# Performance work log

Hardware: AMD Instinct MI355X
Metric: run time of the kernel (lower is better)

## Reference

```python
import jax, jax.numpy as jnp
import numpy as np

NUMERICAL_STABILIZER = 1e-3  # Performer relu_kernel_transformation stabilizer


def _relu_kernel(x):
    # Performer ReLU kernel feature map (no random projection): relu(x) + eps.
    return jax.nn.relu(x) + NUMERICAL_STABILIZER


def setup_inputs() -> dict:
    key = jax.random.key(0)
    kq, kk, kv = jax.random.split(key, 3)
    B, L, D = 8, 32768, 64
    return {
        "queries": jax.random.normal(kq, (B, L, D), dtype=jnp.float32),
        "keys": jax.random.normal(kk, (B, L, D), dtype=jnp.float32),
        "values": jax.random.normal(kv, (B, L, D), dtype=jnp.float32),
        "top_k": 64,
    }


def reference(queries, keys, values, top_k):
    # Kernel feature maps (head dim of 1 in the original is a no-op squeeze).
    q_prime = _relu_kernel(queries)  # [B, L, D]
    k_prime = _relu_kernel(keys)     # [B, L, D]
    # ones[1,L] @ q_prime  ==  column sum over L  -> [B, D]
    reduced_q = jnp.sum(q_prime, axis=1)
    # scores[b, l] = reduced_q[b] . k_prime[b, l]   (attention column sums)
    scores = jnp.einsum("bd,bld->bl", reduced_q, k_prime)  # [B, L]
    # Cutoff = (top_k+1)-th largest score, matching sorted_idxs[:, top_k].
    cutoff = jax.lax.top_k(scores, top_k + 1)[0][:, top_k]  # [B]
    cond = scores > cutoff[:, None]                          # [B, L]
    return jnp.where(cond[:, :, None], values, jnp.zeros_like(values))
```

## Files before the change

kernel.cpp:

```cpp
#include <hip/hip_runtime.h>

#define BB 8
#define LL 32768
#define DD 64

typedef float f4 __attribute__((ext_vector_type(4)));
typedef unsigned long long u64x2 __attribute__((ext_vector_type(2)));


#define OUT_F4 (BB * LL * DD / 4)
#define CHUNKS_Q 64
#define ROWS_Q (LL / CHUNKS_Q)

__global__ __launch_bounds__(256) void k_reduce_q(const float* __restrict__ q,
                                                  double* __restrict__ part,
                                                  float* __restrict__ out) {
    {
        f4 z = (f4)(0.0f);
        f4* oz = (f4*)out + (size_t)blockIdx.x * 4096 + threadIdx.x;
#pragma unroll
        for (int i = 0; i < 16; ++i) oz[i * 256] = z;
    }

    int b     = blockIdx.x >> 6;
    int chunk = blockIdx.x & (CHUNKS_Q - 1);
    int quad  = threadIdx.x & 15;
    int rowg  = threadIdx.x >> 4;

    const f4* qb = (const f4*)(q + (size_t)b * LL * DD);
    const f4* base = qb + (size_t)(chunk * ROWS_Q + rowg) * 16 + quad;

    double a0 = 0.0, a1 = 0.0, a2 = 0.0, a3 = 0.0;
    f4 vb[8];
#pragma unroll
    for (int batch = 0; batch < 4; ++batch) {
#pragma unroll
        for (int j = 0; j < 8; ++j)
            vb[j] = base[(size_t)(batch * 8 + j) * 256];
#pragma unroll
        for (int j = 0; j < 8; ++j) {
            a0 += (double)fmaxf(vb[j].x, 0.0f) + 1e-3;
            a1 += (double)fmaxf(vb[j].y, 0.0f) + 1e-3;
            a2 += (double)fmaxf(vb[j].z, 0.0f) + 1e-3;
            a3 += (double)fmaxf(vb[j].w, 0.0f) + 1e-3;
        }
    }

    __shared__ double lds[16][16][5];
    lds[rowg][quad][0] = a0; lds[rowg][quad][1] = a1;
    lds[rowg][quad][2] = a2; lds[rowg][quad][3] = a3;
    __syncthreads();
    for (int s = 8; s > 0; s >>= 1) {
        if (rowg < s) {
            lds[rowg][quad][0] += lds[rowg + s][quad][0];
            lds[rowg][quad][1] += lds[rowg + s][quad][1];
            lds[rowg][quad][2] += lds[rowg + s][quad][2];
            lds[rowg][quad][3] += lds[rowg + s][quad][3];
        }
        __syncthreads();
    }
    if (rowg == 0) {
        double* pp = part + ((size_t)b * CHUNKS_Q + chunk) * DD;
        pp[quad * 4 + 0] = lds[0][quad][0];
        pp[quad * 4 + 1] = lds[0][quad][1];
        pp[quad * 4 + 2] = lds[0][quad][2];
        pp[quad * 4 + 3] = lds[0][quad][3];
    }
}

__global__ __launch_bounds__(256) void k_scores(const float* __restrict__ k,
                                                const double* __restrict__ part,
                                                double* __restrict__ scores,
                                                float* __restrict__ out) {
    __shared__ double s_part[4][DD];
    __shared__ double s_rq[DD];

    {
        f4 z = (f4)(0.0f);
        f4* oz = (f4*)out + (size_t)(OUT_F4 / 2)
               + (size_t)blockIdx.x * 2048 + threadIdx.x;
#pragma unroll
        for (int i = 0; i < 8; ++i) oz[i * 256] = z;
    }

    const int RPB = 256;
    int b     = blockIdx.x >> 7;
    int chunk = blockIdx.x & 127;

    {
        int d = threadIdx.x & 63;
        int g = threadIdx.x >> 6;
        const double* pp = part + (size_t)b * CHUNKS_Q * DD;
        double acc = 0.0;
#pragma unroll
        for (int j = 0; j < 16; ++j)
            acc += pp[(size_t)(g * 16 + j) * DD + d];
        s_part[g][d] = acc;
    }
    __syncthreads();
    if (threadIdx.x < DD) {
        int d = threadIdx.x;
        s_rq[d] = (s_part[0][d] + s_part[1][d]) + (s_part[2][d] + s_part[3][d]);
    }
    __syncthreads();

    int sub   = threadIdx.x & 15;
    int rowIn = threadIdx.x >> 4;

    double r0 = s_rq[sub * 4 + 0];
    double r1 = s_rq[sub * 4 + 1];
    double r2 = s_rq[sub * 4 + 2];
    double r3 = s_rq[sub * 4 + 3];

    const f4* kb = (const f4*)(k + (size_t)b * LL * DD);
    int l0 = chunk * RPB;
    const f4* base = kb + (size_t)(l0 + rowIn) * 16 + sub;

    f4 vb[8];
    double sv[8];
#pragma unroll
    for (int batch = 0; batch < 2; ++batch) {
#pragma unroll
        for (int i = 0; i < 8; ++i)
            vb[i] = base[(size_t)(batch * 8 + i) * 256];
#pragma unroll
        for (int i = 0; i < 8; ++i) {
            sv[i] = r0 * ((double)fmaxf(vb[i].x, 0.0f) + 1e-3)
                  + r1 * ((double)fmaxf(vb[i].y, 0.0f) + 1e-3)
                  + r2 * ((double)fmaxf(vb[i].z, 0.0f) + 1e-3)
                  + r3 * ((double)fmaxf(vb[i].w, 0.0f) + 1e-3);
        }
#pragma unroll
        for (int i = 0; i < 8; ++i) {
            double s = sv[i];
            s += __shfl_xor(s, 1, 16);
            s += __shfl_xor(s, 2, 16);
            s += __shfl_xor(s, 4, 16);
            s += __shfl_xor(s, 8, 16);
            if (sub == 0)
                scores[(size_t)b * LL + l0 + rowIn + 16 * (batch * 8 + i)] = s;
        }
    }
}

#define NCOPY 16
#define HSTRIDE 257
#define MAXSEL 96
__global__ __launch_bounds__(1024) void k_select_gather(const double* __restrict__ scores,
                                                        const int* __restrict__ topk_p,
                                                        const float* __restrict__ v,
                                                        float* __restrict__ out) {
    const int T = 1024;
    int b   = blockIdx.x;
    int tid = threadIdx.x;

    const u64x2* sb2 = (const u64x2*)(scores + (size_t)b * LL);

    unsigned long long myAnd = ~0ULL, myOr = 0ULL;
#pragma unroll
    for (int batch = 0; batch < 2; ++batch) {
        u64x2 p[8];
#pragma unroll
        for (int j = 0; j < 8; ++j) p[j] = sb2[tid + (batch * 8 + j) * T];
#pragma unroll
        for (int j = 0; j < 8; ++j) { myAnd &= p[j].x & p[j].y; myOr |= p[j].x | p[j].y; }
    }
    __shared__ unsigned long long sAnd[16], sOr[16];
#pragma unroll
    for (int off = 32; off >= 1; off >>= 1) {
        myAnd &= __shfl_down(myAnd, off);
        myOr  |= __shfl_down(myOr, off);
    }
    int wave = tid >> 6;
    if ((tid & 63) == 0) { sAnd[wave] = myAnd; sOr[wave] = myOr; }
    __syncthreads();
    __shared__ unsigned long long bAnd, bOr;
    __shared__ unsigned long long sh_prefix;
    __shared__ int sh_r, sh_digit, sh_newr, sh_cnt, sh_done, sh_ov, sh_cache_ok;
    __shared__ unsigned int hist[NCOPY * HSTRIDE];
    __shared__ unsigned int sWaveTot[4];
    if (tid == 0) {
        unsigned long long a = ~0ULL, o = 0ULL;
#pragma unroll
        for (int w = 0; w < 16; ++w) { a &= sAnd[w]; o |= sOr[w]; }
        bAnd = a; bOr = o;
        sh_prefix = 0ULL; sh_r = topk_p[0]; sh_done = 0; sh_cache_ok = 0;
    }
    __syncthreads();

    int copy = tid & (NCOPY - 1);
    unsigned long long m0 = 0, m1 = 0;
    int mcnt = 0;

    for (int shift = 56; shift >= 0; shift -= 8) {
        if (sh_done) break;

        unsigned int dA = (unsigned int)(bAnd >> shift) & 255u;
        unsigned int dO = (unsigned int)(bOr  >> shift) & 255u;
        if (dA == dO) {
            if (tid == 0) sh_prefix |= ((unsigned long long)dA << shift);
            __syncthreads();
            continue;
        }

        for (int i = tid; i < NCOPY * HSTRIDE; i += T) hist[i] = 0;
        if (tid == 0) sh_ov = 0;
        __syncthreads();

        int r = sh_r;
        unsigned long long prefix = sh_prefix;
        unsigned long long hm = (shift == 56) ? 0ULL : (~0ULL << (shift + 8));
        int usec = sh_cache_ok;

        if (usec) {
            if (mcnt >= 1) atomicAdd(&hist[copy * HSTRIDE + ((unsigned)(m0 >> shift) & 255u)], 1u);
            if (mcnt >= 2) atomicAdd(&hist[copy * HSTRIDE + ((unsigned)(m1 >> shift) & 255u)], 1u);
        } else {
            mcnt = 0;
#pragma unroll
            for (int batch = 0; batch < 2; ++batch) {
                u64x2 p[8];
#pragma unroll
                for (int j = 0; j < 8; ++j) p[j] = sb2[tid + (batch * 8 + j) * T];
#pragma unroll
                for (int j = 0; j < 8; ++j) {
                    unsigned long long ka = p[j].x, kb2 = p[j].y;
                    if ((ka & hm) == prefix) {
                        atomicAdd(&hist[copy * HSTRIDE + ((unsigned)(ka >> shift) & 255u)], 1u);
                        if (mcnt == 0) m0 = ka; else if (mcnt == 1) m1 = ka;
                        ++mcnt;
                    }
                    if ((kb2 & hm) == prefix) {
                        atomicAdd(&hist[copy * HSTRIDE + ((unsigned)(kb2 >> shift) & 255u)], 1u);
                        if (mcnt == 0) m0 = kb2; else if (mcnt == 1) m1 = kb2;
                        ++mcnt;
                    }
                }
            }
            if (mcnt > 2) sh_ov = 1;
        }
        __syncthreads();

        unsigned int suf = 0, sufn = 0;
        if (tid < 256) {
            unsigned int vtot = 0;
#pragma unroll
            for (int c = 0; c < NCOPY; ++c) vtot += hist[c * HSTRIDE + tid];
            unsigned int vv = vtot;
            int lane = tid & 63;
#pragma unroll
            for (int off = 1; off < 64; off <<= 1) {
                unsigned int t = __shfl_down(vv, off);
                if (lane + off < 64) vv += t;
            }
            if (lane == 0) sWaveTot[tid >> 6] = vv;
            suf = vv;
        }
        __syncthreads();
        if (tid < 256) {
            int lane = tid & 63, w = tid >> 6;
            unsigned int add = 0;
#pragma unroll
            for (int ww = 0; ww < 4; ++ww)
                if (ww > w) add += sWaveTot[ww];
            unsigned int nsuf = __shfl_down(suf, 1);
            suf += add;
            sufn = ((lane == 63) ? 0u : nsuf) + add;
            if (suf > (unsigned int)r && sufn <= (unsigned int)r) {
                sh_digit = tid;
                sh_newr  = r - (int)sufn;
                sh_cnt   = (int)(suf - sufn);
            }
        }
        __syncthreads();
        if (tid == 0) {
            sh_prefix |= ((unsigned long long)sh_digit << shift);
            sh_r = sh_newr;
            if (!usec) sh_cache_ok = (sh_ov == 0);
        }
        __syncthreads();

        {
            unsigned int dsel = (unsigned int)sh_digit;
            unsigned long long n0 = 0, n1 = 0;
            int nm = 0;
            if (mcnt >= 1 && (((unsigned)(m0 >> shift) & 255u) == dsel)) { n0 = m0; nm = 1; }
            if (mcnt >= 2 && (((unsigned)(m1 >> shift) & 255u) == dsel)) {
                if (nm == 0) n0 = m1; else n1 = m1;
                ++nm;
            }
            m0 = n0; m1 = n1; mcnt = nm;
        }

        if (sh_cnt == 1 && sh_cache_ok && shift > 0) {
            if (mcnt >= 1) {
                sh_prefix = m0;
                sh_done = 1;
            }
        }
        __syncthreads();
    }

    __shared__ int s_cnt;
    __shared__ int s_idx[MAXSEL];
    if (tid == 0) s_cnt = 0;
    __syncthreads();
    unsigned long long cb = sh_prefix;
#pragma unroll
    for (int batch = 0; batch < 2; ++batch) {
        u64x2 p[8];
#pragma unroll
        for (int j = 0; j < 8; ++j) p[j] = sb2[tid + (batch * 8 + j) * T];
#pragma unroll
        for (int j = 0; j < 8; ++j) {
            int jj = batch * 8 + j;
            if (p[j].x > cb) {
                int slot = atomicAdd(&s_cnt, 1);
                if (slot < MAXSEL) s_idx[slot] = 2 * (tid + jj * T);
            }
            if (p[j].y > cb) {
                int slot = atomicAdd(&s_cnt, 1);
                if (slot < MAXSEL) s_idx[slot] = 2 * (tid + jj * T) + 1;
            }
        }
    }
    __syncthreads();
    int cnt = s_cnt < MAXSEL ? s_cnt : MAXSEL;

    int g      = tid >> 4;
    int lane16 = tid & 15;
    for (int r = g; r < cnt; r += 64) {
        size_t rowOff = ((size_t)b * LL + s_idx[r]) * DD;
        const f4* vrow = (const f4*)(v + rowOff);
        f4*       orow = (f4*)(out + rowOff);
        orow[lane16] = vrow[lane16];
    }
}

extern "C" void kernel_launch(void* const* d_in, const int* in_sizes, int n_in,
                              void* d_out, int out_size, void* d_ws, size_t ws_size,
                              hipStream_t stream) {
    const float* q = (const float*)d_in[0];
    const float* k = (const float*)d_in[1];
    const float* v = (const float*)d_in[2];
    const int* topk = (const int*)d_in[3];
    float* out = (float*)d_out;

    double* part   = (double*)d_ws;
    double* scores = (double*)((char*)d_ws + 262144);

    k_reduce_q<<<BB * CHUNKS_Q, 256, 0, stream>>>(q, part, out);
    k_scores<<<BB * (LL / 256), 256, 0, stream>>>(k, part, scores, out);
    k_select_gather<<<BB, 1024, 0, stream>>>(scores, topk, v, out);
}
```

Before: 61.22 us.

## Add parallel candidate filter kernel before per-batch top-k radix select

```diff
diff --git a/kernel.cpp b/kernel.cpp
--- a/kernel.cpp
+++ b/kernel.cpp
@@ -11,10 +11,22 @@
 #define OUT_F4 (BB * LL * DD / 4)
 #define CHUNKS_Q 64
 #define ROWS_Q (LL / CHUNKS_Q)
+#define CAP 2048
+#define NCOPY 16
+#define HSTRIDE 257
+#define MAXSEL 96
 
 __global__ __launch_bounds__(256) void k_reduce_q(const float* __restrict__ q,
                                                   double* __restrict__ part,
-                                                  float* __restrict__ out) {
+                                                  float* __restrict__ out,
+                                                  unsigned long long* __restrict__ gAnd,
+                                                  unsigned long long* __restrict__ gOr,
+                                                  unsigned int* __restrict__ gcnt) {
+    if (blockIdx.x < BB && threadIdx.x == 0) {
+        gAnd[blockIdx.x] = ~0ULL;
+        gOr[blockIdx.x]  = 0ULL;
+        gcnt[blockIdx.x] = 0u;
+    }
     {
         f4 z = (f4)(0.0f);
         f4* oz = (f4*)out + (size_t)blockIdx.x * 4096 + threadIdx.x;
@@ -71,9 +83,12 @@
 __global__ __launch_bounds__(256) void k_scores(const float* __restrict__ k,
                                                 const double* __restrict__ part,
                                                 double* __restrict__ scores,
-                                                float* __restrict__ out) {
+                                                float* __restrict__ out,
+                                                unsigned long long* __restrict__ gAnd,
+                                                unsigned long long* __restrict__ gOr) {
     __shared__ double s_part[4][DD];
     __shared__ double s_rq[DD];
+    __shared__ unsigned long long sA2[4], sO2[4];
 
     {
         f4 z = (f4)(0.0f);
@@ -116,6 +131,7 @@
     int l0 = chunk * RPB;
     const f4* base = kb + (size_t)(l0 + rowIn) * 16 + sub;
 
+    unsigned long long ma = ~0ULL, mo = 0ULL;
     f4 vb[8];
     double sv[8];
 #pragma unroll
@@ -137,86 +153,268 @@
             s += __shfl_xor(s, 2, 16);
             s += __shfl_xor(s, 4, 16);
             s += __shfl_xor(s, 8, 16);
-            if (sub == 0)
+            if (sub == 0) {
                 scores[(size_t)b * LL + l0 + rowIn + 16 * (batch * 8 + i)] = s;
-        }
+                unsigned long long u = (unsigned long long)__double_as_longlong(s);
+                ma &= u; mo |= u;
+            }
+        }
+    }
+
+#pragma unroll
+    for (int off = 32; off >= 1; off >>= 1) {
+        ma &= __shfl_xor(ma, off);
+        mo |= __shfl_xor(mo, off);
+    }
+    if ((threadIdx.x & 63) == 0) { sA2[threadIdx.x >> 6] = ma; sO2[threadIdx.x >> 6] = mo; }
+    __syncthreads();
+    if (threadIdx.x == 0) {
+        unsigned long long a = sA2[0] & sA2[1] & sA2[2] & sA2[3];
+        unsigned long long o = sO2[0] | sO2[1] | sO2[2] | sO2[3];
+        atomicAnd(&gAnd[b], a);
+        atomicOr(&gOr[b], o);
     }
 }
 
-#define NCOPY 16
-#define HSTRIDE 257
-#define MAXSEL 96
-__global__ __launch_bounds__(1024) void k_select_gather(const double* __restrict__ scores,
-                                                        const int* __restrict__ topk_p,
-                                                        const float* __restrict__ v,
-                                                        float* __restrict__ out) {
+__global__ __launch_bounds__(256) void k_filter(const double* __restrict__ scores,
+                                                const unsigned long long* __restrict__ gAnd,
+                                                const unsigned long long* __restrict__ gOr,
+                                                const int* __restrict__ topk_p,
+                                                unsigned int* __restrict__ gcnt,
+                                                unsigned long long* __restrict__ candKey,
+                                                unsigned int* __restrict__ candIdx) {
+    int b   = blockIdx.x >> 4;
+    int s   = blockIdx.x & 15;
+    int tid = threadIdx.x;
+    unsigned long long A = gAnd[b], O = gOr[b];
+    if (A == O) return;
+
+    int sB = 0;
+    for (int sh = 56; sh >= 0; sh -= 8)
+        if ((((A >> sh) ^ (O >> sh)) & 255ULL) != 0ULL) { sB = sh; break; }
+    int shift2 = (sB >= 3) ? (sB - 3) : 0;
+    unsigned int K1 = (unsigned int)topk_p[0] + 1u;
+
+    const u64x2* sb2 = (const u64x2*)(scores + (size_t)b * LL);
+    u64x2 p[4];
+#pragma unroll
+    for (int j = 0; j < 4; ++j) p[j] = sb2[(size_t)s * 1024 + tid + j * 256];
+
+    __shared__ unsigned int hist[2048];
+    __shared__ unsigned long long sKey[2048];
+    __shared__ unsigned int sIdx[2048];
+    __shared__ unsigned int sW[4];
+    __shared__ unsigned int s_loc, s_base;
+    for (int i = tid; i < 2048; i += 256) hist[i] = 0;
+    if (tid == 0) s_loc = 0;
+    __syncthreads();
+#pragma unroll
+    for (int j = 0; j < 4; ++j) {
+        atomicAdd(&hist[(unsigned)(p[j].x >> shift2) & 2047u], 1u);
+        atomicAdd(&hist[(unsigned)(p[j].y >> shift2) & 2047u], 1u);
+    }
+    __syncthreads();
+
+    unsigned int h[8], sl[8];
+#pragma unroll
+    for (int j = 0; j < 8; ++j) h[j] = hist[tid * 8 + j];
+    unsigned int run = 0;
+#pragma unroll
+    for (int j = 7; j >= 0; --j) { run += h[j]; sl[j] = run; }
+    unsigned int tot = run, vv = tot;
+    int lane = tid & 63;
+#pragma unroll
+    for (int off = 1; off < 64; off <<= 1) {
+        unsigned int t = __shfl_down(vv, off);
+        if (lane + off < 64) vv += t;
+    }
+    if (lane == 0) sW[tid >> 6] = vv;
+    __syncthreads();
+    unsigned int add = 0;
+    int w = tid >> 6;
+#pragma unroll
+    for (int ww = 0; ww < 4; ++ww) if (ww > w) add += sW[ww];
+    unsigned int above = (vv + add) - tot;
+    __syncthreads();
+#pragma unroll
+    for (int j = 0; j < 8; ++j) hist[tid * 8 + j] = above + sl[j];
+    __syncthreads();
+
+#pragma unroll
+    for (int j = 0; j < 4; ++j) {
+        unsigned long long kx = p[j].x;
+        unsigned int dx = (unsigned)(kx >> shift2) & 2047u;
+        if (dx == 2047u || hist[dx + 1] < K1) {
+            unsigned int sl2 = atomicAdd(&s_loc, 1u);
+            sKey[sl2] = kx;
+            sIdx[sl2] = 2u * ((unsigned)s * 1024u + (unsigned)tid + (unsigned)j * 256u);
+        }
+        unsigned long long ky = p[j].y;
+        unsigned int dy = (unsigned)(ky >> shift2) & 2047u;
+        if (dy == 2047u || hist[dy + 1] < K1) {
+            unsigned int sl2 = atomicAdd(&s_loc, 1u);
+            sKey[sl2] = ky;
+            sIdx[sl2] = 2u * ((unsigned)s * 1024u + (unsigned)tid + (unsigned)j * 256u) + 1u;
+        }
+    }
+    __syncthreads();
+    if (tid == 0) s_base = atomicAdd(&gcnt[b], s_loc);
+    __syncthreads();
+    unsigned int nb = s_loc, base2 = s_base;
+    for (unsigned int i = tid; i < nb; i += 256) {
+        unsigned int g = base2 + i;
+        if (g < CAP) {
+            candKey[(size_t)b * CAP + g] = sKey[i];
+            candIdx[(size_t)b * CAP + g] = sIdx[i];
+        }
+    }
+}
+
+#define RADIX_SCAN(RVAR)                                                        \
+    {                                                                           \
+        unsigned int suf = 0, sufn = 0;                                         \
+        if (tid < 256) {                                                        \
+            unsigned int vtot = 0;                                              \
+            _Pragma("unroll")                                                   \
+            for (int c = 0; c < NCOPY; ++c) vtot += hist[c * HSTRIDE + tid];    \
+            unsigned int vv2 = vtot;                                            \
+            int lane2 = tid & 63;                                               \
+            _Pragma("unroll")                                                   \
+            for (int off = 1; off < 64; off <<= 1) {                            \
+                unsigned int t2 = __shfl_down(vv2, off);                        \
+                if (lane2 + off < 64) vv2 += t2;                                \
+            }                                                                   \
+            if (lane2 == 0) sWaveTot[tid >> 6] = vv2;                           \
+            suf = vv2;                                                          \
+        }                                                                       \
+        __syncthreads();                                                        \
+        if (tid < 256) {                                                        \
+            int lane2 = tid & 63, w2 = tid >> 6;                                \
+            unsigned int add2 = 0;                                              \
+            _Pragma("unroll")                                                   \
+            for (int ww = 0; ww < 4; ++ww) if (ww > w2) add2 += sWaveTot[ww];   \
+            unsigned int nsuf = __shfl_down(suf, 1);                            \
+            suf += add2;                                                        \
+            sufn = ((lane2 == 63) ? 0u : nsuf) + add2;                          \
+            if (suf > (unsigned int)(RVAR) && sufn <= (unsigned int)(RVAR)) {   \
+                sh_digit = tid;                                                 \
+                sh_newr  = (RVAR) - (int)sufn;                                  \
+                sh_cnt   = (int)(suf - sufn);                                   \
+            }                                                                   \
+        }                                                                       \
+        __syncthreads();                                                        \
+    }
+
+__global__ __launch_bounds__(1024) void k_select_gather(
+        const double* __restrict__ scores,
+        const unsigned long long* __restrict__ gAnd,
+        const unsigned long long* __restrict__ gOr,
+        const unsigned int* __restrict__ gcnt,
+        const unsigned long long* __restrict__ candKey,
+        const unsigned int* __restrict__ candIdx,
+        const int* __restrict__ topk_p,
+        const float* __restrict__ v,
+        float* __restrict__ out) {
     const int T = 1024;
-    int b   = blockIdx.x;
-    int tid = threadIdx.x;
-
-    const u64x2* sb2 = (const u64x2*)(scores + (size_t)b * LL);
-
-    unsigned long long myAnd = ~0ULL, myOr = 0ULL;
-#pragma unroll
-    for (int batch = 0; batch < 2; ++batch) {
-        u64x2 p[8];
-#pragma unroll
-        for (int j = 0; j < 8; ++j) p[j] = sb2[tid + (batch * 8 + j) * T];
-#pragma unroll
-        for (int j = 0; j < 8; ++j) { myAnd &= p[j].x & p[j].y; myOr |= p[j].x | p[j].y; }
-    }
-    __shared__ unsigned long long sAnd[16], sOr[16];
-#pragma unroll
-    for (int off = 32; off >= 1; off >>= 1) {
-        myAnd &= __shfl_down(myAnd, off);
-        myOr  |= __shfl_down(myOr, off);
-    }
-    int wave = tid >> 6;
-    if ((tid & 63) == 0) { sAnd[wave] = myAnd; sOr[wave] = myOr; }
-    __syncthreads();
-    __shared__ unsigned long long bAnd, bOr;
-    __shared__ unsigned long long sh_prefix;
-    __shared__ int sh_r, sh_digit, sh_newr, sh_cnt, sh_done, sh_ov, sh_cache_ok;
+    int b = blockIdx.x, tid = threadIdx.x;
+    unsigned long long A = gAnd[b], O = gOr[b];
+    if (A == O) return;
+
     __shared__ unsigned int hist[NCOPY * HSTRIDE];
+    __shared__ unsigned long long sA16[16], sO16[16];
     __shared__ unsigned int sWaveTot[4];
-    if (tid == 0) {
-        unsigned long long a = ~0ULL, o = 0ULL;
-#pragma unroll
-        for (int w = 0; w < 16; ++w) { a &= sAnd[w]; o |= sOr[w]; }
-        bAnd = a; bOr = o;
-        sh_prefix = 0ULL; sh_r = topk_p[0]; sh_done = 0; sh_cache_ok = 0;
-    }
-    __syncthreads();
-
-    int copy = tid & (NCOPY - 1);
-    unsigned long long m0 = 0, m1 = 0;
-    int mcnt = 0;
-
-    for (int shift = 56; shift >= 0; shift -= 8) {
-        if (sh_done) break;
-
-        unsigned int dA = (unsigned int)(bAnd >> shift) & 255u;
-        unsigned int dO = (unsigned int)(bOr  >> shift) & 255u;
-        if (dA == dO) {
-            if (tid == 0) sh_prefix |= ((unsigned long long)dA << shift);
-            __syncthreads();
-            continue;
-        }
-
-        for (int i = tid; i < NCOPY * HSTRIDE; i += T) hist[i] = 0;
-        if (tid == 0) sh_ov = 0;
-        __syncthreads();
-
-        int r = sh_r;
-        unsigned long long prefix = sh_prefix;
-        unsigned long long hm = (shift == 56) ? 0ULL : (~0ULL << (shift + 8));
-        int usec = sh_cache_ok;
-
-        if (usec) {
-            if (mcnt >= 1) atomicAdd(&hist[copy * HSTRIDE + ((unsigned)(m0 >> shift) & 255u)], 1u);
-            if (mcnt >= 2) atomicAdd(&hist[copy * HSTRIDE + ((unsigned)(m1 >> shift) & 255u)], 1u);
-        } else {
-            mcnt = 0;
+    __shared__ unsigned long long sh_prefix, cA, cO;
+    __shared__ int sh_r, sh_digit, sh_newr, sh_cnt, sh_done;
+    __shared__ int s_cnt;
+    __shared__ int s_idx[MAXSEL];
+
+    unsigned int n0 = gcnt[b];
+    if (n0 == 0) return;
+
+    if (n0 <= CAP) {
+        bool v0 = tid < (int)n0, v1 = tid + T < (int)n0;
+        unsigned long long c0 = v0 ? candKey[(size_t)b * CAP + tid] : 0ULL;
+        unsigned long long c1 = v1 ? candKey[(size_t)b * CAP + tid + T] : 0ULL;
+        unsigned int i0 = v0 ? candIdx[(size_t)b * CAP + tid] : 0u;
+        unsigned int i1 = v1 ? candIdx[(size_t)b * CAP + tid + T] : 0u;
+
+        unsigned long long ma = ~0ULL, mo = 0ULL;
+        if (v0) { ma &= c0; mo |= c0; }
+        if (v1) { ma &= c1; mo |= c1; }
+#pragma unroll
+        for (int off = 32; off >= 1; off >>= 1) {
+            ma &= __shfl_xor(ma, off);
+            mo |= __shfl_xor(mo, off);
+        }
+        if ((tid & 63) == 0) { sA16[tid >> 6] = ma; sO16[tid >> 6] = mo; }
+        __syncthreads();
+        if (tid == 0) {
+            unsigned long long a = ~0ULL, o = 0ULL;
+#pragma unroll
+            for (int w2 = 0; w2 < 16; ++w2) { a &= sA16[w2]; o |= sO16[w2]; }
+            cA = a; cO = o;
+            sh_prefix = 0ULL; sh_r = topk_p[0]; sh_done = 0;
+        }
+        __syncthreads();
+
+        int copy = tid & (NCOPY - 1);
+        bool f0 = v0, f1 = v1;
+
+        for (int shift = 56; shift >= 0; shift -= 8) {
+            if (sh_done) break;
+            unsigned int dA2 = (unsigned int)(cA >> shift) & 255u;
+            unsigned int dO2 = (unsigned int)(cO >> shift) & 255u;
+            if (dA2 == dO2) {
+                if (tid == 0) sh_prefix |= ((unsigned long long)dA2 << shift);
+                __syncthreads();
+                continue;
+            }
+            for (int i = tid; i < NCOPY * HSTRIDE; i += T) hist[i] = 0;
+            __syncthreads();
+            int r = sh_r;
+            if (f0) atomicAdd(&hist[copy * HSTRIDE + ((unsigned)(c0 >> shift) & 255u)], 1u);
+            if (f1) atomicAdd(&hist[copy * HSTRIDE + ((unsigned)(c1 >> shift) & 255u)], 1u);
+            __syncthreads();
+            RADIX_SCAN(r)
+            if (tid == 0) {
+                sh_prefix |= ((unsigned long long)sh_digit << shift);
+                sh_r = sh_newr;
+            }
+            __syncthreads();
+            unsigned int dsel = (unsigned int)sh_digit;
+            if (f0 && (((unsigned)(c0 >> shift) & 255u) != dsel)) f0 = false;
+            if (f1 && (((unsigned)(c1 >> shift) & 255u) != dsel)) f1 = false;
+            if (sh_cnt == 1) {
+                if (f0)      { sh_prefix = c0; sh_done = 1; }
+                else if (f1) { sh_prefix = c1; sh_done = 1; }
+            }
+            __syncthreads();
+        }
+
+        unsigned long long cb = sh_prefix;
+        if (tid == 0) s_cnt = 0;
+        __syncthreads();
+        if (v0 && c0 > cb) { int sl = atomicAdd(&s_cnt, 1); if (sl < MAXSEL) s_idx[sl] = (int)i0; }
+        if (v1 && c1 > cb) { int sl = atomicAdd(&s_cnt, 1); if (sl < MAXSEL) s_idx[sl] = (int)i1; }
+        __syncthreads();
+    } else {
+        const u64x2* sb2 = (const u64x2*)(scores + (size_t)b * LL);
+        if (tid == 0) { sh_prefix = 0ULL; sh_r = topk_p[0]; }
+        __syncthreads();
+        int copy = tid & (NCOPY - 1);
+        for (int shift = 56; shift >= 0; shift -= 8) {
+            unsigned int dA2 = (unsigned int)(A >> shift) & 255u;
+            unsigned int dO2 = (unsigned int)(O >> shift) & 255u;
+            if (dA2 == dO2) {
+                if (tid == 0) sh_prefix |= ((unsigned long long)dA2 << shift);
+                __syncthreads();
+                continue;
+            }
+            for (int i = tid; i < NCOPY * HSTRIDE; i += T) hist[i] = 0;
+            __syncthreads();
+            unsigned long long prefix = sh_prefix;
+            unsigned long long hm = (shift == 56) ? 0ULL : (~0ULL << (shift + 8));
+            int r = sh_r;
 #pragma unroll
             for (int batch = 0; batch < 2; ++batch) {
                 u64x2 p[8];
@@ -224,113 +422,42 @@
                 for (int j = 0; j < 8; ++j) p[j] = sb2[tid + (batch * 8 + j) * T];
 #pragma unroll
                 for (int j = 0; j < 8; ++j) {
-                    unsigned long long ka = p[j].x, kb2 = p[j].y;
-                    if ((ka & hm) == prefix) {
-                        atomicAdd(&hist[copy * HSTRIDE + ((unsigned)(ka >> shift) & 255u)], 1u);
-                        if (mcnt == 0) m0 = ka; else if (mcnt == 1) m1 = ka;
-                        ++mcnt;
-                    }
-                    if ((kb2 & hm) == prefix) {
-                        atomicAdd(&hist[copy * HSTRIDE + ((unsigned)(kb2 >> shift) & 255u)], 1u);
-                        if (mcnt == 0) m0 = kb2; else if (mcnt == 1) m1 = kb2;
-                        ++mcnt;
-                    }
+                    if ((p[j].x & hm) == prefix)
+                        atomicAdd(&hist[copy * HSTRIDE + ((unsigned)(p[j].x >> shift) & 255u)], 1u);
+                    if ((p[j].y & hm) == prefix)
+                        atomicAdd(&hist[copy * HSTRIDE + ((unsigned)(p[j].y >> shift) & 255u)], 1u);
                 }
             }
-            if (mcnt > 2) sh_ov = 1;
-        }
-        __syncthreads();
-
-        unsigned int suf = 0, sufn = 0;
-        if (tid < 256) {
-            unsigned int vtot = 0;
-#pragma unroll
-            for (int c = 0; c < NCOPY; ++c) vtot += hist[c * HSTRIDE + tid];
-            unsigned int vv = vtot;
-            int lane = tid & 63;
-#pragma unroll
-            for (int off = 1; off < 64; off <<= 1) {
-                unsigned int t = __shfl_down(vv, off);
-                if (lane + off < 64) vv += t;
-            }
-            if (lane == 0) sWaveTot[tid >> 6] = vv;
-            suf = vv;
-        }
-        __syncthreads();
-        if (tid < 256) {
-            int lane = tid & 63, w = tid >> 6;
-            unsigned int add = 0;
-#pragma unroll
-            for (int ww = 0; ww < 4; ++ww)
-                if (ww > w) add += sWaveTot[ww];
-            unsigned int nsuf = __shfl_down(suf, 1);
-            suf += add;
-            sufn = ((lane == 63) ? 0u : nsuf) + add;
-            if (suf > (unsigned int)r && sufn <= (unsigned int)r) {
-                sh_digit = tid;
-                sh_newr  = r - (int)sufn;
-                sh_cnt   = (int)(suf - sufn);
-            }
-        }
-        __syncthreads();
-        if (tid == 0) {
-            sh_prefix |= ((unsigned long long)sh_digit << shift);
-            sh_r = sh_newr;
-            if (!usec) sh_cache_ok = (sh_ov == 0);
-        }
-        __syncthreads();
-
-        {
-            unsigned int dsel = (unsigned int)sh_digit;
-            unsigned long long n0 = 0, n1 = 0;
-            int nm = 0;
-            if (mcnt >= 1 && (((unsigned)(m0 >> shift) & 255u) == dsel)) { n0 = m0; nm = 1; }
-            if (mcnt >= 2 && (((unsigned)(m1 >> shift) & 255u) == dsel)) {
-                if (nm == 0) n0 = m1; else n1 = m1;
-                ++nm;
-            }
-            m0 = n0; m1 = n1; mcnt = nm;
-        }
-
-        if (sh_cnt == 1 && sh_cache_ok && shift > 0) {
-            if (mcnt >= 1) {
-                sh_prefix = m0;
-                sh_done = 1;
-            }
-        }
-        __syncthreads();
-    }
-
-    __shared__ int s_cnt;
-    __shared__ int s_idx[MAXSEL];
-    if (tid == 0) s_cnt = 0;
-    __syncthreads();
-    unsigned long long cb = sh_prefix;
-#pragma unroll
-    for (int batch = 0; batch < 2; ++batch) {
-        u64x2 p[8];
-#pragma unroll
-        for (int j = 0; j < 8; ++j) p[j] = sb2[tid + (batch * 8 + j) * T];
-#pragma unroll
-        for (int j = 0; j < 8; ++j) {
-            int jj = batch * 8 + j;
-            if (p[j].x > cb) {
-                int slot = atomicAdd(&s_cnt, 1);
-                if (slot < MAXSEL) s_idx[slot] = 2 * (tid + jj * T);
-            }
-            if (p[j].y > cb) {
-                int slot = atomicAdd(&s_cnt, 1);
-                if (slot < MAXSEL) s_idx[slot] = 2 * (tid + jj * T) + 1;
-            }
-        }
-    }
-    __syncthreads();
+            __syncthreads();
+            RADIX_SCAN(r)
+            if (tid == 0) {
+                sh_prefix |= ((unsigned long long)sh_digit << shift);
+                sh_r = sh_newr;
+            }
+            __syncthreads();
+        }
+        unsigned long long cb = sh_prefix;
+        if (tid == 0) s_cnt = 0;
+        __syncthreads();
+#pragma unroll
+        for (int batch = 0; batch < 2; ++batch) {
+            u64x2 p[8];
+#pragma unroll
+            for (int j = 0; j < 8; ++j) p[j] = sb2[tid + (batch * 8 + j) * T];
+#pragma unroll
+            for (int j = 0; j < 8; ++j) {
+                int jj = batch * 8 + j;
+                if (p[j].x > cb) { int sl = atomicAdd(&s_cnt, 1); if (sl < MAXSEL) s_idx[sl] = 2 * (tid + jj * T); }
+                if (p[j].y > cb) { int sl = atomicAdd(&s_cnt, 1); if (sl < MAXSEL) s_idx[sl] = 2 * (tid + jj * T) + 1; }
+            }
+        }
+        __syncthreads();
+    }
+
     int cnt = s_cnt < MAXSEL ? s_cnt : MAXSEL;
-
-    int g      = tid >> 4;
-    int lane16 = tid & 15;
-    for (int r = g; r < cnt; r += 64) {
-        size_t rowOff = ((size_t)b * LL + s_idx[r]) * DD;
+    int g = tid >> 4, lane16 = tid & 15;
+    for (int r2 = g; r2 < cnt; r2 += 64) {
+        size_t rowOff = ((size_t)b * LL + s_idx[r2]) * DD;
         const f4* vrow = (const f4*)(v + rowOff);
         f4*       orow = (f4*)(out + rowOff);
         orow[lane16] = vrow[lane16];
@@ -348,8 +475,15 @@
 
     double* part   = (double*)d_ws;
     double* scores = (double*)((char*)d_ws + 262144);
-
-    k_reduce_q<<<BB * CHUNKS_Q, 256, 0, stream>>>(q, part, out);
-    k_scores<<<BB * (LL / 256), 256, 0, stream>>>(k, part, scores, out);
-    k_select_gather<<<BB, 1024, 0, stream>>>(scores, topk, v, out);
+    char* aux = (char*)d_ws + 262144 + 2097152;
+    unsigned long long* gAnd    = (unsigned long long*)aux;
+    unsigned long long* gOr     = (unsigned long long*)(aux + 64);
+    unsigned int*       gcnt    = (unsigned int*)(aux + 128);
+    unsigned long long* candKey = (unsigned long long*)(aux + 256);
+    unsigned int*       candIdx = (unsigned int*)(aux + 256 + (size_t)BB * CAP * 8);
+
+    k_reduce_q<<<BB * CHUNKS_Q, 256, 0, stream>>>(q, part, out, gAnd, gOr, gcnt);
+    k_scores<<<BB * (LL / 256), 256, 0, stream>>>(k, part, scores, out, gAnd, gOr);
+    k_filter<<<BB * 16, 256, 0, stream>>>(scores, gAnd, gOr, topk, gcnt, candKey, candIdx);
+    k_select_gather<<<BB, 1024, 0, stream>>>(scores, gAnd, gOr, gcnt, candKey, candIdx, topk, v, out);
 }
```

Measured after the change: 85.92 us. 40.3% more time.
